# Kernel tuning notes

Measured on AMD Instinct MI355X. Metric: run time of the kernel, lower is better.

## Reference

```python
import jax, jax.numpy as jnp
import numpy as np

B, S, P = 2, 1024, 1024          # batch, new tokens, cached (past) tokens
H, NQ, NKV, D = 4096, 32, 8, 128  # hidden, q heads, kv heads, head dim
G = NQ // NKV                     # GQA group size
SCALE = 1.0 / np.sqrt(D)


def _make_rope(positions, dim, base=10000.0):
    inv = 1.0 / (base ** (np.arange(0, dim, 2, dtype=np.float32) / dim))
    freqs = positions[:, None].astype(np.float32) * inv[None, :]
    emb = np.concatenate([freqs, freqs], axis=-1)  # [S, D]
    return jnp.asarray(np.cos(emb)), jnp.asarray(np.sin(emb))


def setup_inputs() -> dict:
    key = jax.random.key(0)
    ks = jax.random.split(key, 5)
    hidden_states = jax.random.normal(ks[0], (B, S, H), jnp.float32)
    w_qkv = jax.random.normal(ks[1], (H, (NQ + 2 * NKV) * D), jnp.float32) * 0.02
    w_o = jax.random.normal(ks[2], (NQ * D, H), jnp.float32) * 0.02
    cos, sin = _make_rope(np.arange(P, P + S), D)  # new tokens at positions P..P+S-1
    k_cache = jax.random.normal(ks[3], (B, P, NKV, D), jnp.float32)
    v_cache = jax.random.normal(ks[4], (B, P, NKV, D), jnp.float32)
    return dict(hidden_states=hidden_states, w_qkv=w_qkv, w_o=w_o,
                cos=cos, sin=sin, k_cache=k_cache, v_cache=v_cache)


def _rotate_half(x):
    x1, x2 = jnp.split(x, 2, axis=-1)
    return jnp.concatenate([-x2, x1], axis=-1)


def _apply_rope(x, cos, sin):
    # x: [B,S,N,D]; cos/sin: [S,D]
    return x * cos[None, :, None, :] + _rotate_half(x) * sin[None, :, None, :]


def reference(hidden_states, w_qkv, w_o, cos, sin, k_cache, v_cache):
    # fused QKV projection
    qkv = hidden_states @ w_qkv                       # [B,S,(NQ+2*NKV)*D]
    q, k, v = jnp.split(qkv, [NQ * D, (NQ + NKV) * D], axis=-1)
    q = q.reshape(B, S, NQ, D)
    k = k.reshape(B, S, NKV, D)
    v = v.reshape(B, S, NKV, D)
    # inline RoPE on q and k
    q = _apply_rope(q, cos, sin)
    k = _apply_rope(k, cos, sin)
    # append new k/v to the KV cache (quant_bits=0 path: fp cache)
    k_all = jnp.concatenate([k_cache, k], axis=1)     # [B,T,NKV,D], T = P+S
    v_all = jnp.concatenate([v_cache, v], axis=1)
    # GQA attention: group q heads per kv head
    qg = q.reshape(B, S, NKV, G, D)
    scores = jnp.einsum('bsngd,btnd->bngst', qg, k_all) * SCALE  # [B,NKV,G,S,T]
    # causal mask offset by cache length: new token s sees t <= s + P
    t_idx = jnp.arange(P + S)
    s_idx = jnp.arange(S)
    mask = t_idx[None, :] <= (s_idx[:, None] + P)      # [S,T]
    neg = jnp.asarray(jnp.finfo(scores.dtype).min, scores.dtype)
    scores = jnp.where(mask[None, None, None], scores, neg)
    probs = jax.nn.softmax(scores, axis=-1)
    out = jnp.einsum('bngst,btnd->bsngd', probs, v_all).reshape(B, S, NQ * D)
    return out @ w_o                                   # [B,S,H]
```

## Files before the change

### kernel.cpp

```cpp
#include <hip/hip_runtime.h>
#include <hip/hip_bf16.h>
#include <cstdint>
#include <cstddef>

#define B_    2
#define S_    1024
#define P_    1024
#define T_    2048
#define H_    4096
#define NQ_   32
#define NKV_  8
#define D_    128
#define QKVN_ 6144
#define SCALE_ 0.08838834764831845f

typedef unsigned short u16;
typedef short  bf16x8 __attribute__((ext_vector_type(8)));
typedef float  f32x4  __attribute__((ext_vector_type(4)));

__device__ __forceinline__ float bf2f(u16 u) {
  union { unsigned u; float f; } x; x.u = ((unsigned)u) << 16; return x.f;
}
__device__ __forceinline__ u16 f2bf(float f) {
  union { float f; unsigned u; } x; x.f = f;
  unsigned r = (x.u + 0x7fffu + ((x.u >> 16) & 1u)) >> 16;
  return (u16)r;
}

__device__ __forceinline__ void gload16(const void* g, void* l) {
  __builtin_amdgcn_global_load_lds(
      (const __attribute__((address_space(1))) unsigned int*)g,
      (__attribute__((address_space(3))) unsigned int*)l, 16, 0, 0);
}

__global__ void k_f32_to_bf16(const float* __restrict__ in, u16* __restrict__ out, int n4) {
  int i = blockIdx.x * blockDim.x + threadIdx.x;
  if (i >= n4) return;
  float4 v = ((const float4*)in)[i];
  union { u16 s[4]; uint2 v; } o;
  o.s[0] = f2bf(v.x); o.s[1] = f2bf(v.y); o.s[2] = f2bf(v.z); o.s[3] = f2bf(v.w);
  ((uint2*)out)[i] = o.v;
}

__global__ void k_wtrans(const float* __restrict__ w, u16* __restrict__ wt, int K, int N) {
  __shared__ __align__(16) u16 tile[64][66];
  const int n0 = blockIdx.x * 64;
  const int k0 = blockIdx.y * 64;
  const int tid = threadIdx.x;
  const int c = tid & 63;
  const int r4 = tid >> 6;
#pragma unroll
  for (int i = 0; i < 16; ++i) {
    int rr = r4 * 16 + i;
    tile[rr][c] = f2bf(w[(size_t)(k0 + rr) * N + n0 + c]);
  }
  __syncthreads();
#pragma unroll
  for (int i = 0; i < 16; ++i) {
    int rr = r4 * 16 + i;
    wt[(size_t)(n0 + rr) * K + k0 + c] = tile[c][rr];
  }
}

template<bool BF16OUT>
__global__ __launch_bounds__(256, 2)
void k_gemm(const u16* __restrict__ A, const u16* __restrict__ Bt,
            void* __restrict__ Cv, int M, int N, int K) {
  __shared__ __align__(16) u16 As[128 * 64];
  __shared__ __align__(16) u16 Bs[128 * 64];
  const int tid = threadIdx.x;
  const int lane = tid & 63;
  const int wv = tid >> 6;
  const int wm = wv >> 1, wn = wv & 1;
  const int m0 = blockIdx.y * 128;
  const int n0 = blockIdx.x * 128;
  const int l15 = lane & 15, l4 = lane >> 4;

  f32x4 acc[4][4] = {};
  const int nk = K >> 6;
  int srow[4], scol[4];
#pragma unroll
  for (int i = 0; i < 4; ++i) {
    int chunk = tid + i * 256;
    srow[i] = chunk >> 3;
    scol[i] = (chunk & 7) ^ (srow[i] & 7);
  }
  for (int kt = 0; kt < nk; ++kt) {
    __syncthreads();
#pragma unroll
    for (int i = 0; i < 4; ++i) {
      int chunk = tid + i * 256;
      gload16(A  + (size_t)(m0 + srow[i]) * K + kt * 64 + scol[i] * 8, &As[chunk * 8]);
      gload16(Bt + (size_t)(n0 + srow[i]) * K + kt * 64 + scol[i] * 8, &Bs[chunk * 8]);
    }
    __syncthreads();
    bf16x8 af[4][2], bfr[4][2];
#pragma unroll
    for (int mt = 0; mt < 4; ++mt) {
      int r = wm * 64 + mt * 16 + l15;
#pragma unroll
      for (int ks = 0; ks < 2; ++ks) {
        int cc = (ks * 4 + l4) ^ (r & 7);
        af[mt][ks] = *(const bf16x8*)(&As[r * 64 + cc * 8]);
      }
    }
#pragma unroll
    for (int nt = 0; nt < 4; ++nt) {
      int r = wn * 64 + nt * 16 + l15;
#pragma unroll
      for (int ks = 0; ks < 2; ++ks) {
        int cc = (ks * 4 + l4) ^ (r & 7);
        bfr[nt][ks] = *(const bf16x8*)(&Bs[r * 64 + cc * 8]);
      }
    }
#pragma unroll
    for (int mt = 0; mt < 4; ++mt)
#pragma unroll
      for (int nt = 0; nt < 4; ++nt)
#pragma unroll
        for (int ks = 0; ks < 2; ++ks)
          acc[mt][nt] = __builtin_amdgcn_mfma_f32_16x16x32_bf16(
              af[mt][ks], bfr[nt][ks], acc[mt][nt], 0, 0, 0);
  }
#pragma unroll
  for (int mt = 0; mt < 4; ++mt)
#pragma unroll
    for (int nt = 0; nt < 4; ++nt)
#pragma unroll
      for (int i = 0; i < 4; ++i) {
        int row = m0 + wm * 64 + mt * 16 + l4 * 4 + i;
        int col = n0 + wn * 64 + nt * 16 + l15;
        size_t off = (size_t)row * N + col;
        if (BF16OUT) ((u16*)Cv)[off] = f2bf(acc[mt][nt][i]);
        else         ((float*)Cv)[off] = acc[mt][nt][i];
      }
}

__global__ void k_rope_scatter(const u16* __restrict__ qkv,
                               const float* __restrict__ cosb, const float* __restrict__ sinb,
                               const float* __restrict__ kcache,
                               u16* __restrict__ Q, u16* __restrict__ Kall) {
  const int gsz = gridDim.x * blockDim.x;
  const int i0 = blockIdx.x * blockDim.x + threadIdx.x;
  for (int i = i0; i < B_ * S_ * NQ_ * 64; i += gsz) {
    int d = i & 63, hh = (i >> 6) & 31, s = (i >> 11) & 1023, b = i >> 21;
    const u16* row = qkv + (size_t)(b * S_ + s) * QKVN_ + hh * D_;
    float x1 = bf2f(row[d]), x2 = bf2f(row[d + 64]);
    float c = cosb[s * D_ + d], sn = sinb[s * D_ + d];
    u16* q = Q + (size_t)((b * NQ_ + hh) * S_ + s) * D_;
    q[d]      = f2bf((x1 * c - x2 * sn) * SCALE_);
    q[d + 64] = f2bf((x2 * c + x1 * sn) * SCALE_);
  }
  for (int i = i0; i < B_ * S_ * NKV_ * 64; i += gsz) {
    int d = i & 63, kh = (i >> 6) & 7, s = (i >> 9) & 1023, b = i >> 19;
    const u16* row = qkv + (size_t)(b * S_ + s) * QKVN_ + NQ_ * D_ + kh * D_;
    float x1 = bf2f(row[d]), x2 = bf2f(row[d + 64]);
    float c = cosb[s * D_ + d], sn = sinb[s * D_ + d];
    u16* kd = Kall + (size_t)((b * NKV_ + kh) * T_ + P_ + s) * D_;
    kd[d]      = f2bf(x1 * c - x2 * sn);
    kd[d + 64] = f2bf(x2 * c + x1 * sn);
  }
  for (int i = i0; i < B_ * P_ * NKV_ * D_; i += gsz) {
    int d = i & 127, kh = (i >> 7) & 7, t = (i >> 10) & 1023, b = i >> 20;
    float x = kcache[(size_t)((b * P_ + t) * NKV_ + kh) * D_ + d];
    Kall[(size_t)((b * NKV_ + kh) * T_ + t) * D_ + d] = f2bf(x);
  }
}

__global__ void k_vbuild(const u16* __restrict__ qkv, const float* __restrict__ vcache,
                         u16* __restrict__ Vt) {
  __shared__ __align__(16) u16 tile[64][66];
  const int t0 = blockIdx.x * 64;
  const int d0 = blockIdx.y * 64;
  const int bkh = blockIdx.z;
  const int b = bkh >> 3, kh = bkh & 7;
  const int tid = threadIdx.x;
  const int c = tid & 63, r4 = tid >> 6;
#pragma unroll
  for (int i = 0; i < 16; ++i) {
    int rr = r4 * 16 + i;
    int t = t0 + rr;
    float x;
    if (t < P_) x = vcache[(size_t)((b * P_ + t) * NKV_ + kh) * D_ + d0 + c];
    else        x = bf2f(qkv[(size_t)(b * S_ + (t - P_)) * QKVN_ + (NQ_ + NKV_) * D_ + kh * D_ + d0 + c]);
    tile[rr][c] = f2bf(x);
  }
  __syncthreads();
  u16* out = Vt + ((size_t)(b * NKV_ + kh) * D_ + d0) * T_ + t0;
#pragma unroll
  for (int i = 0; i < 16; ++i) {
    int rr = r4 * 16 + i;
    out[(size_t)rr * T_ + c] = tile[c][rr];
  }
}

__global__ __launch_bounds__(256, 2)
void k_attn(const u16* __restrict__ Q, const u16* __restrict__ Kall,
            const u16* __restrict__ Vt, u16* __restrict__ O) {
  __shared__ __align__(16) u16 Ks[2][64 * 128];
  __shared__ __align__(16) u16 Vs[2][128 * 64];
  __shared__ __align__(16) u16 Ps[4][32 * 64];
  const int sb = blockIdx.x;
  const int h  = blockIdx.y;
  const int b  = blockIdx.z;
  const int kh = h >> 2;
  const int tid = threadIdx.x;
  const int lane = tid & 63, wv = tid >> 6;
  const int l15 = lane & 15, l4 = lane >> 4;
  const int s0 = sb * 128;
  const int rowbase = s0 + wv * 32;

  const u16* kbase = Kall + (size_t)(b * NKV_ + kh) * T_ * D_;
  const u16* vbase = Vt   + (size_t)(b * NKV_ + kh) * D_ * T_;
  const int ntiles = min(32, 2 * sb + 18);

  int kr[4], kc[4], vr[4], vc[4];
#pragma unroll
  for (int i = 0; i < 4; ++i) {
    int chunk = tid + i * 256;
    kr[i] = chunk >> 4; kc[i] = (chunk & 15) ^ (kr[i] & 7);
    vr[i] = chunk >> 3; vc[i] = (chunk & 7)  ^ (vr[i] & 7);
  }
  auto stage = [&](int buf, int t0) {
#pragma unroll
    for (int i = 0; i < 4; ++i) {
      int chunk = tid + i * 256;
      gload16(kbase + (size_t)(t0 + kr[i]) * D_ + kc[i] * 8, &Ks[buf][chunk * 8]);
      gload16(vbase + (size_t)vr[i] * T_ + t0 + vc[i] * 8,  &Vs[buf][chunk * 8]);
    }
  };

  const u16* qbase = Q + (size_t)(b * NQ_ + h) * S_ * D_;
  bf16x8 qf[2][4];
#pragma unroll
  for (int mt = 0; mt < 2; ++mt)
#pragma unroll
    for (int ks = 0; ks < 4; ++ks)
      qf[mt][ks] = *(const bf16x8*)(qbase + (size_t)(rowbase + mt * 16 + l15) * D_ + ks * 32 + l4 * 8);

  f32x4 acco[2][8] = {};
  float mrun[2][4], lrun[2][4];
#pragma unroll
  for (int mt = 0; mt < 2; ++mt)
#pragma unroll
    for (int i = 0; i < 4; ++i) { mrun[mt][i] = -1e30f; lrun[mt][i] = 0.f; }

  stage(0, 0);

  for (int tt = 0; tt < ntiles; ++tt) {
    const int cur = tt & 1;
    const int t0 = tt * 64;
    if (tt + 1 < ntiles) {
      stage(cur ^ 1, (tt + 1) * 64);
      asm volatile("s_waitcnt vmcnt(8)" ::: "memory");
    } else {
      asm volatile("s_waitcnt vmcnt(0)" ::: "memory");
    }
    __builtin_amdgcn_sched_barrier(0);
    __builtin_amdgcn_s_barrier();
    __builtin_amdgcn_sched_barrier(0);

    f32x4 accs[2][4] = {};
    __builtin_amdgcn_s_setprio(1);
#pragma unroll
    for (int tb = 0; tb < 4; ++tb) {
      int r = tb * 16 + l15;
#pragma unroll
      for (int ks = 0; ks < 4; ++ks) {
        int cc = (ks * 4 + l4) ^ (r & 7);
        bf16x8 kf = *(const bf16x8*)(&Ks[cur][r * 128 + cc * 8]);
#pragma unroll
        for (int mt = 0; mt < 2; ++mt)
          accs[mt][tb] = __builtin_amdgcn_mfma_f32_16x16x32_bf16(qf[mt][ks], kf, accs[mt][tb], 0, 0, 0);
      }
    }
    __builtin_amdgcn_s_setprio(0);
    if (tt >= 2 * sb + 16) {
#pragma unroll
      for (int mt = 0; mt < 2; ++mt)
#pragma unroll
        for (int tb = 0; tb < 4; ++tb)
#pragma unroll
          for (int i = 0; i < 4; ++i) {
            int srow = rowbase + mt * 16 + l4 * 4 + i;
            int tcol = t0 + tb * 16 + l15;
            if (tcol > srow + P_) accs[mt][tb][i] = -1e30f;
          }
    }
#pragma unroll
    for (int mt = 0; mt < 2; ++mt) {
      float vmax[4];
#pragma unroll
      for (int i = 0; i < 4; ++i) {
        float v = fmaxf(fmaxf(accs[mt][0][i], accs[mt][1][i]),
                        fmaxf(accs[mt][2][i], accs[mt][3][i]));
        v = fmaxf(v, __shfl_xor(v, 1));
        v = fmaxf(v, __shfl_xor(v, 2));
        v = fmaxf(v, __shfl_xor(v, 4));
        v = fmaxf(v, __shfl_xor(v, 8));
        vmax[i] = v;
      }
      bool ok = true;
#pragma unroll
      for (int i = 0; i < 4; ++i) ok = ok && (vmax[i] <= mrun[mt][i] + 8.f);
      if (!__all(ok)) {
#pragma unroll
        for (int i = 0; i < 4; ++i) {
          float mn = fmaxf(mrun[mt][i], vmax[i]);
          float al = __expf(mrun[mt][i] - mn);
          mrun[mt][i] = mn;
          lrun[mt][i] *= al;
#pragma unroll
          for (int db = 0; db < 8; ++db)
            acco[mt][db][i] *= al;
        }
      }
      float rs[4] = {0.f, 0.f, 0.f, 0.f};
#pragma unroll
      for (int tb = 0; tb < 4; ++tb)
#pragma unroll
        for (int i = 0; i < 4; ++i) {
          float p = __expf(accs[mt][tb][i] - mrun[mt][i]);
          accs[mt][tb][i] = p;
          rs[i] += p;
        }
#pragma unroll
      for (int i = 0; i < 4; ++i) {
        rs[i] += __shfl_xor(rs[i], 1);
        rs[i] += __shfl_xor(rs[i], 2);
        rs[i] += __shfl_xor(rs[i], 4);
        rs[i] += __shfl_xor(rs[i], 8);
        lrun[mt][i] += rs[i];
      }
#pragma unroll
      for (int tb = 0; tb < 4; ++tb)
#pragma unroll
        for (int i = 0; i < 4; ++i) {
          int r = mt * 16 + l4 * 4 + i;
          int col = tb * 16 + l15;
          int cc = (col >> 3) ^ (r & 7);
          Ps[wv][r * 64 + cc * 8 + (col & 7)] = f2bf(accs[mt][tb][i]);
        }
    }
    __builtin_amdgcn_s_setprio(1);
#pragma unroll
    for (int ks = 0; ks < 2; ++ks) {
      bf16x8 pf[2];
#pragma unroll
      for (int mt = 0; mt < 2; ++mt) {
        int r = mt * 16 + l15;
        int cc = (ks * 4 + l4) ^ (r & 7);
        pf[mt] = *(const bf16x8*)(&Ps[wv][r * 64 + cc * 8]);
      }
#pragma unroll
      for (int db = 0; db < 8; ++db) {
        int r = db * 16 + l15;
        int cc = (ks * 4 + l4) ^ (r & 7);
        bf16x8 vf = *(const bf16x8*)(&Vs[cur][r * 64 + cc * 8]);
#pragma unroll
        for (int mt = 0; mt < 2; ++mt)
          acco[mt][db] = __builtin_amdgcn_mfma_f32_16x16x32_bf16(pf[mt], vf, acco[mt][db], 0, 0, 0);
      }
    }
    __builtin_amdgcn_s_setprio(0);
    __builtin_amdgcn_sched_barrier(0);
    __builtin_amdgcn_s_barrier();
    __builtin_amdgcn_sched_barrier(0);
  }
#pragma unroll
  for (int mt = 0; mt < 2; ++mt)
#pragma unroll
    for (int db = 0; db < 8; ++db)
#pragma unroll
      for (int i = 0; i < 4; ++i) {
        int srow = rowbase + mt * 16 + l4 * 4 + i;
        int d = db * 16 + l15;
        float o = acco[mt][db][i] / lrun[mt][i];
        O[(size_t)(b * S_ + srow) * (NQ_ * D_) + h * D_ + d] = f2bf(o);
      }
}

extern "C" void kernel_launch(void* const* d_in, const int* in_sizes, int n_in,
                              void* d_out, int out_size, void* d_ws, size_t ws_size,
                              hipStream_t stream) {
  const float* hidden = (const float*)d_in[0];
  const float* w_qkv  = (const float*)d_in[1];
  const float* w_o    = (const float*)d_in[2];
  const float* cosb   = (const float*)d_in[3];
  const float* sinb   = (const float*)d_in[4];
  const float* kc     = (const float*)d_in[5];
  const float* vc     = (const float*)d_in[6];
  float* out = (float*)d_out;

  char* ws = (char*)d_ws;
  u16* wqkvt = (u16*)(ws + 0);
  u16* hid   = (u16*)(ws + 50331648);
  u16* qkv   = (u16*)(ws + 67108864);
  u16* wot   = (u16*)(ws + 50331648);
  u16* qrope = (u16*)(ws + 92274688);
  u16* kall  = (u16*)(ws + 109051904);
  u16* vallt = (u16*)(ws + 117440512);
  u16* attno = (u16*)(ws + 125829120);

  k_wtrans<<<dim3(QKVN_ / 64, H_ / 64), 256, 0, stream>>>(w_qkv, wqkvt, H_, QKVN_);
  k_f32_to_bf16<<<(B_ * S_ * H_ / 4 + 255) / 256, 256, 0, stream>>>(hidden, hid, B_ * S_ * H_ / 4);
  k_gemm<true><<<dim3(QKVN_ / 128, (B_ * S_) / 128), 256, 0, stream>>>(
      hid, wqkvt, qkv, B_ * S_, QKVN_, H_);
  k_rope_scatter<<<2048, 256, 0, stream>>>(qkv, cosb, sinb, kc, qrope, kall);
  k_vbuild<<<dim3(T_ / 64, D_ / 64, B_ * NKV_), 256, 0, stream>>>(qkv, vc, vallt);
  k_wtrans<<<dim3(H_ / 64, H_ / 64), 256, 0, stream>>>(w_o, wot, H_, H_);
  k_attn<<<dim3(S_ / 128, NQ_, B_), 256, 0, stream>>>(qrope, kall, vallt, attno);
  k_gemm<false><<<dim3(H_ / 128, (B_ * S_) / 128), 256, 0, stream>>>(
      attno, wot, out, B_ * S_, H_, H_);
}
```

Before: 555.3 us.

## Rewrite attention kernel with 32x32x16 MFMA and transposed S to keep P in registers

The flash-attention kernel moves from 16x16x32 to 32x32x16 bf16 MFMA and computes S transposed (K as the A operand), so each lane owns a single query row. Row max and row sum then need only one cross-half shuffle. P is packed to bf16 with v_cvt_pk_bf16_f32 and rearranged with lane shuffles, which removes the Ps shared-memory round trip before the PV MFMA. The rescale factors and final 1/l are broadcast through a small LDS buffer, and there is no explicit barrier between that write and the following reads, which could be a correctness risk.

```diff
diff --git a/kernel.cpp b/kernel.cpp
--- a/kernel.cpp
+++ b/kernel.cpp
@@ -15,8 +15,10 @@
 #define SCALE_ 0.08838834764831845f
 
 typedef unsigned short u16;
+typedef unsigned int   u32;
 typedef short  bf16x8 __attribute__((ext_vector_type(8)));
 typedef float  f32x4  __attribute__((ext_vector_type(4)));
+typedef float  f32x16 __attribute__((ext_vector_type(16)));
 
 __device__ __forceinline__ float bf2f(u16 u) {
   union { unsigned u; float f; } x; x.u = ((unsigned)u) << 16; return x.f;
@@ -25,6 +27,11 @@
   union { float f; unsigned u; } x; x.f = f;
   unsigned r = (x.u + 0x7fffu + ((x.u >> 16) & 1u)) >> 16;
   return (u16)r;
+}
+__device__ __forceinline__ u32 cvtpk_bf16(float lo, float hi) {
+  u32 r;
+  asm("v_cvt_pk_bf16_f32 %0, %1, %2" : "=v"(r) : "v"(lo), "v"(hi));
+  return r;
 }
 
 __device__ __forceinline__ void gload16(const void* g, void* l) {
@@ -199,16 +206,17 @@
             const u16* __restrict__ Vt, u16* __restrict__ O) {
   __shared__ __align__(16) u16 Ks[2][64 * 128];
   __shared__ __align__(16) u16 Vs[2][128 * 64];
-  __shared__ __align__(16) u16 Ps[4][32 * 64];
+  __shared__ float bcast[4 * 32];
   const int sb = blockIdx.x;
   const int h  = blockIdx.y;
   const int b  = blockIdx.z;
   const int kh = h >> 2;
   const int tid = threadIdx.x;
   const int lane = tid & 63, wv = tid >> 6;
-  const int l15 = lane & 15, l4 = lane >> 4;
+  const int l31 = lane & 31, hi = lane >> 5;
   const int s0 = sb * 128;
   const int rowbase = s0 + wv * 32;
+  const int qrow = rowbase + l31;
 
   const u16* kbase = Kall + (size_t)(b * NKV_ + kh) * T_ * D_;
   const u16* vbase = Vt   + (size_t)(b * NKV_ + kh) * D_ * T_;
@@ -230,20 +238,14 @@
     }
   };
 
-  const u16* qbase = Q + (size_t)(b * NQ_ + h) * S_ * D_;
-  bf16x8 qf[2][4];
-#pragma unroll
-  for (int mt = 0; mt < 2; ++mt)
-#pragma unroll
-    for (int ks = 0; ks < 4; ++ks)
-      qf[mt][ks] = *(const bf16x8*)(qbase + (size_t)(rowbase + mt * 16 + l15) * D_ + ks * 32 + l4 * 8);
-
-  f32x4 acco[2][8] = {};
-  float mrun[2][4], lrun[2][4];
-#pragma unroll
-  for (int mt = 0; mt < 2; ++mt)
-#pragma unroll
-    for (int i = 0; i < 4; ++i) { mrun[mt][i] = -1e30f; lrun[mt][i] = 0.f; }
+  const u16* qbase = Q + (size_t)(b * NQ_ + h) * S_ * D_ + (size_t)qrow * D_;
+  bf16x8 qf[8];
+#pragma unroll
+  for (int ds_ = 0; ds_ < 8; ++ds_)
+    qf[ds_] = *(const bf16x8*)(qbase + ds_ * 16 + hi * 8);
+
+  f32x16 acco[4] = {};
+  float mrun = -1e30f, lrun = 0.f;
 
   stage(0, 0);
 
@@ -260,124 +262,111 @@
     __builtin_amdgcn_s_barrier();
     __builtin_amdgcn_sched_barrier(0);
 
-    f32x4 accs[2][4] = {};
+    f32x16 accs[2] = {};
     __builtin_amdgcn_s_setprio(1);
 #pragma unroll
-    for (int tb = 0; tb < 4; ++tb) {
-      int r = tb * 16 + l15;
-#pragma unroll
-      for (int ks = 0; ks < 4; ++ks) {
-        int cc = (ks * 4 + l4) ^ (r & 7);
+    for (int tb = 0; tb < 2; ++tb) {
+      int r = tb * 32 + l31;
+#pragma unroll
+      for (int ds_ = 0; ds_ < 8; ++ds_) {
+        int cc = (ds_ * 2 + hi) ^ (r & 7);
         bf16x8 kf = *(const bf16x8*)(&Ks[cur][r * 128 + cc * 8]);
-#pragma unroll
-        for (int mt = 0; mt < 2; ++mt)
-          accs[mt][tb] = __builtin_amdgcn_mfma_f32_16x16x32_bf16(qf[mt][ks], kf, accs[mt][tb], 0, 0, 0);
+        accs[tb] = __builtin_amdgcn_mfma_f32_32x32x16_bf16(kf, qf[ds_], accs[tb], 0, 0, 0);
       }
     }
     __builtin_amdgcn_s_setprio(0);
+
     if (tt >= 2 * sb + 16) {
 #pragma unroll
-      for (int mt = 0; mt < 2; ++mt)
-#pragma unroll
-        for (int tb = 0; tb < 4; ++tb)
-#pragma unroll
-          for (int i = 0; i < 4; ++i) {
-            int srow = rowbase + mt * 16 + l4 * 4 + i;
-            int tcol = t0 + tb * 16 + l15;
-            if (tcol > srow + P_) accs[mt][tb][i] = -1e30f;
-          }
-    }
-#pragma unroll
-    for (int mt = 0; mt < 2; ++mt) {
-      float vmax[4];
-#pragma unroll
-      for (int i = 0; i < 4; ++i) {
-        float v = fmaxf(fmaxf(accs[mt][0][i], accs[mt][1][i]),
-                        fmaxf(accs[mt][2][i], accs[mt][3][i]));
-        v = fmaxf(v, __shfl_xor(v, 1));
-        v = fmaxf(v, __shfl_xor(v, 2));
-        v = fmaxf(v, __shfl_xor(v, 4));
-        v = fmaxf(v, __shfl_xor(v, 8));
-        vmax[i] = v;
-      }
-      bool ok = true;
-#pragma unroll
-      for (int i = 0; i < 4; ++i) ok = ok && (vmax[i] <= mrun[mt][i] + 8.f);
-      if (!__all(ok)) {
-#pragma unroll
-        for (int i = 0; i < 4; ++i) {
-          float mn = fmaxf(mrun[mt][i], vmax[i]);
-          float al = __expf(mrun[mt][i] - mn);
-          mrun[mt][i] = mn;
-          lrun[mt][i] *= al;
-#pragma unroll
-          for (int db = 0; db < 8; ++db)
-            acco[mt][db][i] *= al;
+      for (int tb = 0; tb < 2; ++tb)
+#pragma unroll
+        for (int reg = 0; reg < 16; ++reg) {
+          int kv = t0 + tb * 32 + (reg & 3) + 8 * (reg >> 2) + 4 * hi;
+          if (kv > qrow + P_) accs[tb][reg] = -1e30f;
         }
-      }
-      float rs[4] = {0.f, 0.f, 0.f, 0.f};
-#pragma unroll
-      for (int tb = 0; tb < 4; ++tb)
-#pragma unroll
-        for (int i = 0; i < 4; ++i) {
-          float p = __expf(accs[mt][tb][i] - mrun[mt][i]);
-          accs[mt][tb][i] = p;
-          rs[i] += p;
+    }
+
+    float m = accs[0][0];
+#pragma unroll
+    for (int reg = 1; reg < 16; ++reg) m = fmaxf(m, accs[0][reg]);
+#pragma unroll
+    for (int reg = 0; reg < 16; ++reg) m = fmaxf(m, accs[1][reg]);
+    m = fmaxf(m, __shfl_xor(m, 32));
+
+    if (!__all(m <= mrun + 8.f)) {
+      float mn = fmaxf(mrun, m);
+      float al = __expf(mrun - mn);
+      mrun = mn; lrun *= al;
+      if (hi == 0) bcast[wv * 32 + l31] = al;
+      float alq[16];
+#pragma unroll
+      for (int reg = 0; reg < 16; ++reg)
+        alq[reg] = bcast[wv * 32 + (reg & 3) + 8 * (reg >> 2) + 4 * hi];
+#pragma unroll
+      for (int dblk = 0; dblk < 4; ++dblk)
+#pragma unroll
+        for (int reg = 0; reg < 16; ++reg)
+          acco[dblk][reg] *= alq[reg];
+    }
+
+    float rs = 0.f;
+#pragma unroll
+    for (int tb = 0; tb < 2; ++tb)
+#pragma unroll
+      for (int reg = 0; reg < 16; ++reg) {
+        float p = __expf(accs[tb][reg] - mrun);
+        accs[tb][reg] = p;
+        rs += p;
+      }
+    lrun += rs + __shfl_xor(rs, 32);
+
+    __builtin_amdgcn_s_setprio(1);
+#pragma unroll
+    for (int tb = 0; tb < 2; ++tb) {
+#pragma unroll
+      for (int half = 0; half < 2; ++half) {
+        const int bx = half * 8;
+        u32 xa = cvtpk_bf16(accs[tb][bx + 0], accs[tb][bx + 1]);
+        u32 xb = cvtpk_bf16(accs[tb][bx + 2], accs[tb][bx + 3]);
+        u32 ya = cvtpk_bf16(accs[tb][bx + 4], accs[tb][bx + 5]);
+        u32 yb = cvtpk_bf16(accs[tb][bx + 6], accs[tb][bx + 7]);
+        u32 sxa = __shfl_xor(xa, 32), sxb = __shfl_xor(xb, 32);
+        u32 sya = __shfl_xor(ya, 32), syb = __shfl_xor(yb, 32);
+        union { u32 w[4]; bf16x8 v; } pa;
+        pa.w[0] = hi ? sya : xa;
+        pa.w[1] = hi ? syb : xb;
+        pa.w[2] = hi ? ya  : sxa;
+        pa.w[3] = hi ? yb  : sxb;
+        const int ks = tb * 2 + half;
+#pragma unroll
+        for (int dblk = 0; dblk < 4; ++dblk) {
+          int r2 = dblk * 32 + l31;
+          int cc = (ks * 2 + hi) ^ (r2 & 7);
+          bf16x8 vfr = *(const bf16x8*)(&Vs[cur][r2 * 64 + cc * 8]);
+          acco[dblk] = __builtin_amdgcn_mfma_f32_32x32x16_bf16(pa.v, vfr, acco[dblk], 0, 0, 0);
         }
-#pragma unroll
-      for (int i = 0; i < 4; ++i) {
-        rs[i] += __shfl_xor(rs[i], 1);
-        rs[i] += __shfl_xor(rs[i], 2);
-        rs[i] += __shfl_xor(rs[i], 4);
-        rs[i] += __shfl_xor(rs[i], 8);
-        lrun[mt][i] += rs[i];
-      }
-#pragma unroll
-      for (int tb = 0; tb < 4; ++tb)
-#pragma unroll
-        for (int i = 0; i < 4; ++i) {
-          int r = mt * 16 + l4 * 4 + i;
-          int col = tb * 16 + l15;
-          int cc = (col >> 3) ^ (r & 7);
-          Ps[wv][r * 64 + cc * 8 + (col & 7)] = f2bf(accs[mt][tb][i]);
-        }
-    }
-    __builtin_amdgcn_s_setprio(1);
-#pragma unroll
-    for (int ks = 0; ks < 2; ++ks) {
-      bf16x8 pf[2];
-#pragma unroll
-      for (int mt = 0; mt < 2; ++mt) {
-        int r = mt * 16 + l15;
-        int cc = (ks * 4 + l4) ^ (r & 7);
-        pf[mt] = *(const bf16x8*)(&Ps[wv][r * 64 + cc * 8]);
-      }
-#pragma unroll
-      for (int db = 0; db < 8; ++db) {
-        int r = db * 16 + l15;
-        int cc = (ks * 4 + l4) ^ (r & 7);
-        bf16x8 vf = *(const bf16x8*)(&Vs[cur][r * 64 + cc * 8]);
-#pragma unroll
-        for (int mt = 0; mt < 2; ++mt)
-          acco[mt][db] = __builtin_amdgcn_mfma_f32_16x16x32_bf16(pf[mt], vf, acco[mt][db], 0, 0, 0);
       }
     }
     __builtin_amdgcn_s_setprio(0);
+
     __builtin_amdgcn_sched_barrier(0);
     __builtin_amdgcn_s_barrier();
     __builtin_amdgcn_sched_barrier(0);
   }
-#pragma unroll
-  for (int mt = 0; mt < 2; ++mt)
-#pragma unroll
-    for (int db = 0; db < 8; ++db)
-#pragma unroll
-      for (int i = 0; i < 4; ++i) {
-        int srow = rowbase + mt * 16 + l4 * 4 + i;
-        int d = db * 16 + l15;
-        float o = acco[mt][db][i] / lrun[mt][i];
-        O[(size_t)(b * S_ + srow) * (NQ_ * D_) + h * D_ + d] = f2bf(o);
-      }
+
+  if (hi == 0) bcast[wv * 32 + l31] = 1.0f / lrun;
+  float linv[16];
+#pragma unroll
+  for (int reg = 0; reg < 16; ++reg)
+    linv[reg] = bcast[wv * 32 + (reg & 3) + 8 * (reg >> 2) + 4 * hi];
+#pragma unroll
+  for (int dblk = 0; dblk < 4; ++dblk)
+#pragma unroll
+    for (int reg = 0; reg < 16; ++reg) {
+      int q = rowbase + (reg & 3) + 8 * (reg >> 2) + 4 * hi;
+      O[(size_t)(b * S_ + q) * (NQ_ * D_) + h * D_ + dblk * 32 + l31] =
+          f2bf(acco[dblk][reg] * linv[reg]);
+    }
 }
 
 extern "C" void kernel_launch(void* const* d_in, const int* in_sizes, int n_in,
```

Result: faster. 514.8 us (-7.3%).
